# Optimization experiments

Hardware: AMD Instinct MI355X
Metric: run time of the kernel (lower is better)

The kernel has to match this reference:

```python
import jax, jax.numpy as jnp
import numpy as np

N = 8192      # n_nodes
F = 512       # input feature dim
MLP = 512     # mlp_channels
C = 256       # output channels
H = 2         # MLP layers
KPI = 10      # power iterations
ALPHA = 0.1   # teleport probability


def setup_inputs() -> dict:
    key = jax.random.key(0)
    ks = jax.random.split(key, 10)
    features = jax.random.normal(ks[0], (N, F), dtype=jnp.float32)
    # dense normalized-adjacency surrogate: nonnegative, rows ~ sum to 1
    fltr = jax.random.uniform(ks[1], (N, N), dtype=jnp.float32) * (2.0 / N)
    s = 1.0 / np.sqrt(F)
    W_mlp0 = jax.random.normal(ks[2], (F, MLP), dtype=jnp.float32) * s
    b_mlp0 = jnp.zeros((MLP,), dtype=jnp.float32)
    W_mlp1 = jax.random.normal(ks[3], (MLP, MLP), dtype=jnp.float32) * (1.0 / np.sqrt(MLP))
    b_mlp1 = jnp.zeros((MLP,), dtype=jnp.float32)
    W_out = jax.random.normal(ks[4], (MLP, C), dtype=jnp.float32) * (1.0 / np.sqrt(MLP))
    b_out = jnp.zeros((C,), dtype=jnp.float32)
    return {"features": features, "fltr": fltr,
            "W_mlp0": W_mlp0, "b_mlp0": b_mlp0,
            "W_mlp1": W_mlp1, "b_mlp1": b_mlp1,
            "W_out": W_out, "b_out": b_out}


def reference(features, fltr, W_mlp0, b_mlp0, W_mlp1, b_mlp1, W_out, b_out):
    # MLP stage: per layer -> X = relu( A @ (X W + b) )   (dropout_rate = 0)
    x = features
    for W, b in ((W_mlp0, b_mlp0), (W_mlp1, b_mlp1)):
        x = jnp.matmul(fltr, jnp.matmul(x, W) + b)  # [N, MLP]
        x = jax.nn.relu(x)
    # output projection
    z0 = jnp.matmul(x, W_out) + b_out  # [N, C]
    # K-step APPNP power iteration: Z <- (1-alpha) A Z + alpha Z0
    def step(z, _):
        z = (1.0 - ALPHA) * jnp.matmul(fltr, z) + ALPHA * z0
        return z, None
    z, _ = jax.lax.scan(step, z0, None, length=KPI)
    return jax.nn.softmax(z, axis=-1)
```

## Files before the change

kernel.cpp:

```cpp
#include <hip/hip_runtime.h>

typedef unsigned short u16;
typedef __attribute__((ext_vector_type(8))) short bf16x8;
typedef __attribute__((ext_vector_type(4))) float f32x4;

__device__ __forceinline__ float bf2f(u16 u) {
    union { unsigned i; float f; } v; v.i = ((unsigned)u) << 16; return v.f;
}
__device__ __forceinline__ u16 f2bf(float f) {
    union { float f; unsigned i; } v; v.f = f;
    unsigned r = v.i + 0x7FFFu + ((v.i >> 16) & 1u);
    return (u16)(r >> 16);
}

#define GL2LDS(g, l) __builtin_amdgcn_global_load_lds(                         \
    (const __attribute__((address_space(1))) void*)(g),                        \
    (__attribute__((address_space(3))) void*)(l), 16, 0, 0)

template<int EPI, int AFP32>
__global__ __launch_bounds__(256, 4)
void gemm_bt(const void* __restrict__ Ap, int lda,
             const u16* __restrict__ Bt, int ldb,
             int KB,
             void* __restrict__ outp,
             const void* __restrict__ aux,
             int ldout, int NC)
{
    __shared__ u16 aL[128 * 64];
    __shared__ u16 bL[128 * 64];

    const int t = threadIdx.x;
    const int wid = t >> 6, lane = t & 63;
    const int quad = lane >> 4, l15 = lane & 15, l7 = lane & 7;
    const int m0 = blockIdx.x * 128, n0 = blockIdx.y * 128;
    const int sk = blockIdx.z;
    const int k0 = sk * KB * 64;

    f32x4 acc[4][4];
    const f32x4 z4 = {0.f, 0.f, 0.f, 0.f};
#pragma unroll
    for (int i = 0; i < 4; ++i)
#pragma unroll
        for (int j = 0; j < 4; ++j) acc[i][j] = z4;

    const int wm = (wid >> 1) * 64, wn = (wid & 1) * 64;

    if (AFP32 == 0) {
        const char* pa[4]; const char* pb[4]; int lo[4];
#pragma unroll
        for (int i = 0; i < 4; ++i) {
            int flat = i * 4096 + wid * 1024 + lane * 16;
            int row  = flat >> 7;
            int csrc = ((flat >> 4) & 7) ^ (row & 7);
            pa[i] = (const char*)Ap + ((size_t)(m0 + row) * lda + k0) * 2 + csrc * 16;
            pb[i] = (const char*)Bt + ((size_t)(n0 + row) * ldb + k0) * 2 + csrc * 16;
            lo[i] = i * 4096 + wid * 1024;
        }
        for (int kb = 0; kb < KB; ++kb) {
#pragma unroll
            for (int i = 0; i < 4; ++i) GL2LDS(pa[i], (char*)aL + lo[i]);
#pragma unroll
            for (int i = 0; i < 4; ++i) GL2LDS(pb[i], (char*)bL + lo[i]);
#pragma unroll
            for (int i = 0; i < 4; ++i) { pa[i] += 128; pb[i] += 128; }
            __syncthreads();
#pragma unroll
            for (int ks = 0; ks < 2; ++ks) {
                const int cr = ((ks * 4 + quad) ^ l7) * 8;
                bf16x8 av[4], bv[4];
#pragma unroll
                for (int mi = 0; mi < 4; ++mi)
                    av[mi] = *(const bf16x8*)(aL + (wm + mi * 16 + l15) * 64 + cr);
#pragma unroll
                for (int ni = 0; ni < 4; ++ni)
                    bv[ni] = *(const bf16x8*)(bL + (wn + ni * 16 + l15) * 64 + cr);
#pragma unroll
                for (int mi = 0; mi < 4; ++mi)
#pragma unroll
                    for (int ni = 0; ni < 4; ++ni)
                        acc[mi][ni] = __builtin_amdgcn_mfma_f32_16x16x32_bf16(
                            av[mi], bv[ni], acc[mi][ni], 0, 0, 0);
            }
            __syncthreads();
        }
    } else {
        for (int kb = 0; kb < KB; ++kb) {
            const int kbase = k0 + kb * 64;
#pragma unroll
            for (int i = 0; i < 4; ++i) {
                int flat = i * 4096 + t * 16;
                int row  = flat >> 7;
                int col  = (flat & 127) >> 1;
                bf16x8 v = *(const bf16x8*)(Bt + (size_t)(n0 + row) * ldb + kbase + col);
                *(bf16x8*)(bL + row * 64 + col) = v;
            }
            const float* Af = (const float*)Ap;
#pragma unroll
            for (int j = 0; j < 8; ++j) {
                int f = j * 256 + t;
                int r = f >> 4, c = (f & 15) * 4;
                float4 v = *(const float4*)(Af + (size_t)(m0 + r) * lda + kbase + c);
                ushort4 o;
                o.x = f2bf(v.x); o.y = f2bf(v.y);
                o.z = f2bf(v.z); o.w = f2bf(v.w);
                *(ushort4*)(aL + r * 64 + c) = o;
            }
            __syncthreads();
#pragma unroll
            for (int ks = 0; ks < 2; ++ks) {
                const int cr = (ks * 4 + quad) * 8;
                bf16x8 av[4], bv[4];
#pragma unroll
                for (int mi = 0; mi < 4; ++mi)
                    av[mi] = *(const bf16x8*)(aL + (wm + mi * 16 + l15) * 64 + cr);
#pragma unroll
                for (int ni = 0; ni < 4; ++ni)
                    bv[ni] = *(const bf16x8*)(bL + (wn + ni * 16 + l15) * 64 + cr);
#pragma unroll
                for (int mi = 0; mi < 4; ++mi)
#pragma unroll
                    for (int ni = 0; ni < 4; ++ni)
                        acc[mi][ni] = __builtin_amdgcn_mfma_f32_16x16x32_bf16(
                            av[mi], bv[ni], acc[mi][ni], 0, 0, 0);
            }
            __syncthreads();
        }
    }

    if (EPI == 0) {
#pragma unroll
        for (int ni = 0; ni < 4; ++ni) {
            int n = n0 + wn + ni * 16 + l15;
            float bvv = ((const float*)aux)[n];
            u16* ob = (u16*)outp + (size_t)n * ldout;
#pragma unroll
            for (int mi = 0; mi < 4; ++mi) {
                int m = m0 + wm + mi * 16 + quad * 4;
                ushort4 o;
                o.x = f2bf(acc[mi][ni][0] + bvv);
                o.y = f2bf(acc[mi][ni][1] + bvv);
                o.z = f2bf(acc[mi][ni][2] + bvv);
                o.w = f2bf(acc[mi][ni][3] + bvv);
                *(ushort4*)(ob + m) = o;
            }
        }
    } else if (EPI == 2) {
#pragma unroll
        for (int ni = 0; ni < 4; ++ni) {
            int n = n0 + wn + ni * 16 + l15;
            u16* ob = (u16*)outp + ((size_t)(sk * NC + n)) * 8192;
#pragma unroll
            for (int mi = 0; mi < 4; ++mi) {
                int m = m0 + wm + mi * 16 + quad * 4;
                ushort4 o;
                o.x = f2bf(acc[mi][ni][0]);
                o.y = f2bf(acc[mi][ni][1]);
                o.z = f2bf(acc[mi][ni][2]);
                o.w = f2bf(acc[mi][ni][3]);
                *(ushort4*)(ob + m) = o;
            }
        }
    } else if (EPI == 3) {
#pragma unroll
        for (int ni = 0; ni < 4; ++ni) {
            int n = n0 + wn + ni * 16 + l15;
            const u16* zrow = (const u16*)aux + (size_t)n * 8192;
            u16* ob = (u16*)outp + (size_t)n * ldout;
#pragma unroll
            for (int mi = 0; mi < 4; ++mi) {
                int m = m0 + wm + mi * 16 + quad * 4;
                ushort4 z0 = *(const ushort4*)(zrow + m);
                ushort4 o;
                o.x = f2bf(0.9f * acc[mi][ni][0] + 0.1f * bf2f(z0.x));
                o.y = f2bf(0.9f * acc[mi][ni][1] + 0.1f * bf2f(z0.y));
                o.z = f2bf(0.9f * acc[mi][ni][2] + 0.1f * bf2f(z0.z));
                o.w = f2bf(0.9f * acc[mi][ni][3] + 0.1f * bf2f(z0.w));
                *(ushort4*)(ob + m) = o;
            }
        }
    } else {
        u16* ob = (u16*)outp;
#pragma unroll
        for (int mi = 0; mi < 4; ++mi) {
            int m = m0 + wm + mi * 16 + quad * 4;
#pragma unroll
            for (int ni = 0; ni < 4; ++ni) {
                int n = n0 + wn + ni * 16 + l15;
#pragma unroll
                for (int r = 0; r < 4; ++r)
                    ob[(size_t)(m + r) * ldout + n] = f2bf(fmaxf(acc[mi][ni][r], 0.0f));
            }
        }
    }
}

__global__ __launch_bounds__(256)
void cvt_f2b_k(const float* __restrict__ in, u16* __restrict__ out, long n4)
{
    long i = (long)blockIdx.x * 256 + threadIdx.x;
    long stride = (long)gridDim.x * 256;
    for (; i < n4; i += stride) {
        float4 v = ((const float4*)in)[i];
        ushort4 o;
        o.x = f2bf(v.x); o.y = f2bf(v.y); o.z = f2bf(v.z); o.w = f2bf(v.w);
        ((ushort4*)out)[i] = o;
    }
}

__global__ __launch_bounds__(256)
void transpose_cvt_k(const float* __restrict__ in, u16* __restrict__ out,
                     int R, int C)
{
    __shared__ u16 tile[32][33];
    int tx = threadIdx.x, ty = threadIdx.y;
    int x = blockIdx.x * 32 + tx;
    int y0 = blockIdx.y * 32 + ty;
#pragma unroll
    for (int j = 0; j < 32; j += 8)
        tile[ty + j][tx] = f2bf(in[(size_t)(y0 + j) * C + x]);
    __syncthreads();
    int x2 = blockIdx.y * 32 + tx;
    int y2 = blockIdx.x * 32 + ty;
#pragma unroll
    for (int j = 0; j < 32; j += 8)
        out[(size_t)(y2 + j) * R + x2] = tile[tx][ty + j];
}

template<int S>
__global__ __launch_bounds__(256)
void combine_bias_k(const u16* __restrict__ part, const float* __restrict__ bias,
                    u16* __restrict__ out, long NROW)
{
    const size_t Sz = (size_t)NROW * 8192;
    size_t e = ((size_t)blockIdx.x * 256 + threadIdx.x) * 4;
    int n = (int)(e >> 13);
    float b = bias[n];
    ushort4 p0 = *(const ushort4*)(part + e);
    float sx = bf2f(p0.x), sy = bf2f(p0.y), sz = bf2f(p0.z), sw = bf2f(p0.w);
#pragma unroll
    for (int i = 1; i < S; ++i) {
        ushort4 v = *(const ushort4*)(part + (size_t)i * Sz + e);
        sx += bf2f(v.x); sy += bf2f(v.y); sz += bf2f(v.z); sw += bf2f(v.w);
    }
    ushort4 o;
    o.x = f2bf(sx + b); o.y = f2bf(sy + b);
    o.z = f2bf(sz + b); o.w = f2bf(sw + b);
    *(ushort4*)(out + e) = o;
}

template<int S>
__global__ __launch_bounds__(256)
void combine_mlp_k(const u16* __restrict__ part, u16* __restrict__ y)
{
    __shared__ u16 L[64][68];
    const int t = threadIdx.x;
    const int mb = blockIdx.x * 64;
    const int nb = blockIdx.y * 64;
    const size_t Sz = (size_t)512 * 8192;
#pragma unroll
    for (int i = 0; i < 4; ++i) {
        int flat = i * 256 + t;
        int nl = flat >> 4;
        int mq = flat & 15;
        const u16* p0 = part + (size_t)(nb + nl) * 8192 + mb + mq * 4;
        ushort4 a4 = *(const ushort4*)p0;
        float ax = bf2f(a4.x), ay = bf2f(a4.y), az = bf2f(a4.z), aw = bf2f(a4.w);
#pragma unroll
        for (int s = 1; s < S; ++s) {
            ushort4 v = *(const ushort4*)(p0 + (size_t)s * Sz);
            ax += bf2f(v.x); ay += bf2f(v.y); az += bf2f(v.z); aw += bf2f(v.w);
        }
        ushort4 o;
        o.x = f2bf(fmaxf(ax, 0.f)); o.y = f2bf(fmaxf(ay, 0.f));
        o.z = f2bf(fmaxf(az, 0.f)); o.w = f2bf(fmaxf(aw, 0.f));
        *(ushort4*)&L[nl][mq * 4] = o;
    }
    __syncthreads();
#pragma unroll
    for (int i = 0; i < 4; ++i) {
        int flat = i * 256 + t;
        int ml  = flat >> 4;
        int nl4 = (flat & 15) * 4;
        ushort4 o;
        o.x = L[nl4 + 0][ml]; o.y = L[nl4 + 1][ml];
        o.z = L[nl4 + 2][ml]; o.w = L[nl4 + 3][ml];
        *(ushort4*)(y + (size_t)(mb + ml) * 512 + nb + nl4) = o;
    }
}

template<int S>
__global__ __launch_bounds__(256)
void combine_iter_k(const u16* __restrict__ part, const u16* __restrict__ z0T,
                    u16* __restrict__ zT)
{
    const size_t Sz = (size_t)256 * 8192;
    size_t e = ((size_t)blockIdx.x * 256 + threadIdx.x) * 4;
    ushort4 p0 = *(const ushort4*)(part + e);
    float ax = bf2f(p0.x), ay = bf2f(p0.y), az = bf2f(p0.z), aw = bf2f(p0.w);
#pragma unroll
    for (int s = 1; s < S; ++s) {
        ushort4 v = *(const ushort4*)(part + (size_t)s * Sz + e);
        ax += bf2f(v.x); ay += bf2f(v.y); az += bf2f(v.z); aw += bf2f(v.w);
    }
    ushort4 z0 = *(const ushort4*)(z0T + e);
    ushort4 o;
    o.x = f2bf(0.9f * ax + 0.1f * bf2f(z0.x));
    o.y = f2bf(0.9f * ay + 0.1f * bf2f(z0.y));
    o.z = f2bf(0.9f * az + 0.1f * bf2f(z0.z));
    o.w = f2bf(0.9f * aw + 0.1f * bf2f(z0.w));
    *(ushort4*)(zT + e) = o;
}

__global__ __launch_bounds__(256)
void softmax_k(const u16* __restrict__ zT, float* __restrict__ out)
{
    __shared__ u16 L[64][260];
    const int t = threadIdx.x;
    const int m0 = blockIdx.x * 64;
    const int tx = t & 15, ty = t >> 4;
#pragma unroll
    for (int i = 0; i < 16; ++i) {
        int n = i * 16 + ty;
        ushort4 v = *(const ushort4*)(zT + (size_t)n * 8192 + m0 + tx * 4);
        L[tx * 4 + 0][n] = v.x; L[tx * 4 + 1][n] = v.y;
        L[tx * 4 + 2][n] = v.z; L[tx * 4 + 3][n] = v.w;
    }
    __syncthreads();
    const int wid = t >> 6, lane = t & 63;
    for (int r = 0; r < 16; ++r) {
        int mm = wid * 16 + r;
        ushort4 u = *(const ushort4*)(&L[mm][lane * 4]);
        float f0 = bf2f(u.x), f1 = bf2f(u.y), f2 = bf2f(u.z), f3 = bf2f(u.w);
        float mx = fmaxf(fmaxf(f0, f1), fmaxf(f2, f3));
#pragma unroll
        for (int off = 32; off > 0; off >>= 1) mx = fmaxf(mx, __shfl_xor(mx, off));
        float e0 = __expf(f0 - mx), e1 = __expf(f1 - mx);
        float e2 = __expf(f2 - mx), e3 = __expf(f3 - mx);
        float s = e0 + e1 + e2 + e3;
#pragma unroll
        for (int off = 32; off > 0; off >>= 1) s += __shfl_xor(s, off);
        float inv = 1.0f / s;
        float4 o;
        o.x = e0 * inv; o.y = e1 * inv; o.z = e2 * inv; o.w = e3 * inv;
        *(float4*)(out + (size_t)(m0 + mm) * 256 + lane * 4) = o;
    }
}

extern "C" void kernel_launch(void* const* d_in, const int* in_sizes, int n_in,
                              void* d_out, int out_size, void* d_ws, size_t ws_size,
                              hipStream_t stream)
{
    const float* features = (const float*)d_in[0];
    const float* fltr     = (const float*)d_in[1];
    const float* W0       = (const float*)d_in[2];
    const float* b0       = (const float*)d_in[3];
    const float* W1       = (const float*)d_in[4];
    const float* b1       = (const float*)d_in[5];
    const float* Wo       = (const float*)d_in[6];
    const float* bo       = (const float*)d_in[7];

    dim3 tb(32, 8);

    char* p = (char*)d_ws;
    u16* fB  = (u16*)p;  p += (size_t)8192 * 512 * 2;
    u16* W0T = (u16*)p;  p += (size_t)512 * 512 * 2;
    u16* W1T = (u16*)p;  p += (size_t)512 * 512 * 2;
    u16* WoT = (u16*)p;  p += (size_t)256 * 512 * 2;
    u16* z0T = (u16*)p;  p += (size_t)256 * 8192 * 2;
    u16* zA  = (u16*)p;  p += (size_t)256 * 8192 * 2;
    u16* zB  = (u16*)p;  p += (size_t)256 * 8192 * 2;
    u16* tT  = (u16*)p;  p += (size_t)512 * 8192 * 2;
    u16* y   = (u16*)p;  p += (size_t)8192 * 512 * 2;
    u16* part = (u16*)p; p += (size_t)4 * 512 * 8192 * 2;
    size_t base_need = (size_t)(p - (char*)d_ws);
    u16* fltrB = (u16*)p;
    size_t full_need = base_need + (size_t)8192 * 8192 * 2;

    if (ws_size >= full_need) {
        cvt_f2b_k<<<2048, 256, 0, stream>>>(fltr, fltrB, (long)8192 * 8192 / 4);
        cvt_f2b_k<<<512, 256, 0, stream>>>(features, fB, (long)8192 * 512 / 4);
        transpose_cvt_k<<<dim3(16, 16), tb, 0, stream>>>(W0, W0T, 512, 512);
        transpose_cvt_k<<<dim3(16, 16), tb, 0, stream>>>(W1, W1T, 512, 512);
        transpose_cvt_k<<<dim3(8, 16),  tb, 0, stream>>>(Wo, WoT, 512, 256);

        gemm_bt<0, 0><<<dim3(64, 4, 1), 256, 0, stream>>>(fB, 512, W0T, 512, 8,
                                                          tT, b0, 8192, 0);
        gemm_bt<2, 0><<<dim3(64, 4, 2), 256, 0, stream>>>(fltrB, 8192, tT, 8192,
                                                          64, part, nullptr, 0, 512);
        combine_mlp_k<2><<<dim3(128, 8), 256, 0, stream>>>(part, y);
        gemm_bt<0, 0><<<dim3(64, 4, 1), 256, 0, stream>>>(y, 512, W1T, 512, 8,
                                                          tT, b1, 8192, 0);
        gemm_bt<2, 0><<<dim3(64, 4, 2), 256, 0, stream>>>(fltrB, 8192, tT, 8192,
                                                          64, part, nullptr, 0, 512);
        combine_mlp_k<2><<<dim3(128, 8), 256, 0, stream>>>(part, y);
        gemm_bt<0, 0><<<dim3(64, 2, 1), 256, 0, stream>>>(y, 512, WoT, 512, 8,
                                                          z0T, bo, 8192, 0);
        const u16* src = z0T;
        for (int it = 0; it < 10; ++it) {
            u16* dst = (it & 1) ? zB : zA;
            gemm_bt<2, 0><<<dim3(64, 2, 4), 256, 0, stream>>>(fltrB, 8192, src,
                                                              8192, 32, part,
                                                              nullptr, 0, 256);
            combine_iter_k<4><<<2048, 256, 0, stream>>>(part, z0T, dst);
            src = dst;
        }
        softmax_k<<<128, 256, 0, stream>>>(src, (float*)d_out);
    } else if (ws_size >= base_need) {
        cvt_f2b_k<<<512, 256, 0, stream>>>(features, fB, (long)8192 * 512 / 4);
        transpose_cvt_k<<<dim3(16, 16), tb, 0, stream>>>(W0, W0T, 512, 512);
        transpose_cvt_k<<<dim3(16, 16), tb, 0, stream>>>(W1, W1T, 512, 512);
        transpose_cvt_k<<<dim3(8, 16),  tb, 0, stream>>>(Wo, WoT, 512, 256);

        gemm_bt<2, 0><<<dim3(64, 4, 2), 256, 0, stream>>>(fB, 512, W0T, 512, 4,
                                                          part, nullptr, 0, 512);
        combine_bias_k<2><<<4096, 256, 0, stream>>>(part, b0, tT, 512);
        gemm_bt<2, 1><<<dim3(64, 4, 4), 256, 0, stream>>>(fltr, 8192, tT, 8192,
                                                          32, part, nullptr, 0, 512);
        combine_mlp_k<4><<<dim3(128, 8), 256, 0, stream>>>(part, y);
        gemm_bt<2, 0><<<dim3(64, 4, 2), 256, 0, stream>>>(y, 512, W1T, 512, 4,
                                                          part, nullptr, 0, 512);
        combine_bias_k<2><<<4096, 256, 0, stream>>>(part, b1, tT, 512);
        gemm_bt<2, 1><<<dim3(64, 4, 4), 256, 0, stream>>>(fltr, 8192, tT, 8192,
                                                          32, part, nullptr, 0, 512);
        combine_mlp_k<4><<<dim3(128, 8), 256, 0, stream>>>(part, y);
        gemm_bt<2, 0><<<dim3(64, 2, 4), 256, 0, stream>>>(y, 512, WoT, 512, 2,
                                                          part, nullptr, 0, 256);
        combine_bias_k<4><<<2048, 256, 0, stream>>>(part, bo, z0T, 256);
        const u16* src = z0T;
        for (int it = 0; it < 10; ++it) {
            u16* dst = (it & 1) ? zB : zA;
            gemm_bt<2, 1><<<dim3(64, 2, 8), 256, 0, stream>>>(fltr, 8192, src,
                                                              8192, 16, part,
                                                              nullptr, 0, 256);
            combine_iter_k<8><<<2048, 256, 0, stream>>>(part, z0T, dst);
            src = dst;
        }
        softmax_k<<<128, 256, 0, stream>>>(src, (float*)d_out);
    } else {
        char* w = (char*)d_ws;
        u16* fW0T = (u16*)w;  w += (size_t)512 * 512 * 2;
        u16* fW1T = (u16*)w;  w += (size_t)512 * 512 * 2;
        u16* fWoT = (u16*)w;  w += (size_t)256 * 512 * 2;
        u16* fz0T = (u16*)w;  w += (size_t)256 * 8192 * 2;
        char* rb = w;
        u16* ftT = (u16*)rb;
        u16* fy  = (u16*)(rb + (size_t)512 * 8192 * 2);
        u16* fzA = (u16*)rb;
        u16* fzB = (u16*)(rb + (size_t)256 * 8192 * 2);

        transpose_cvt_k<<<dim3(16, 16), tb, 0, stream>>>(W0, fW0T, 512, 512);
        transpose_cvt_k<<<dim3(16, 16), tb, 0, stream>>>(W1, fW1T, 512, 512);
        transpose_cvt_k<<<dim3(8, 16),  tb, 0, stream>>>(Wo, fWoT, 512, 256);
        gemm_bt<0, 1><<<dim3(64, 4), 256, 0, stream>>>(features, 512, fW0T, 512, 8,
                                                       ftT, b0, 8192, 0);
        gemm_bt<1, 1><<<dim3(64, 4), 256, 0, stream>>>(fltr, 8192, ftT, 8192, 128,
                                                       fy, nullptr, 512, 0);
        gemm_bt<0, 0><<<dim3(64, 4), 256, 0, stream>>>(fy, 512, fW1T, 512, 8,
                                                       ftT, b1, 8192, 0);
        gemm_bt<1, 1><<<dim3(64, 4), 256, 0, stream>>>(fltr, 8192, ftT, 8192, 128,
                                                       fy, nullptr, 512, 0);
        gemm_bt<0, 0><<<dim3(64, 2), 256, 0, stream>>>(fy, 512, fWoT, 512, 8,
                                                       fz0T, bo, 8192, 0);
        const u16* src = fz0T;
        for (int it = 0; it < 10; ++it) {
            u16* dst = (it & 1) ? fzB : fzA;
            gemm_bt<3, 1><<<dim3(64, 2), 256, 0, stream>>>(fltr, 8192, src, 8192,
                                                           128, dst, fz0T, 8192, 0);
            src = dst;
        }
        softmax_k<<<128, 256, 0, stream>>>(src, (float*)d_out);
    }
}
```

Measured before the change: 1.115 ms.

## Add 256x256-tile 8-wave GEMM with phased LDS pipeline for adjacency matmuls

After: 1.057 ms. 5.1% less time.

```diff
diff --git a/kernel.cpp b/kernel.cpp
--- a/kernel.cpp
+++ b/kernel.cpp
@@ -193,6 +193,125 @@
         }
     }
 }
+
+#define PHASE_MFMA(MH)                                                        \
+    asm volatile("s_waitcnt lgkmcnt(0)" ::: "memory");                        \
+    __builtin_amdgcn_sched_barrier(0);                                        \
+    __builtin_amdgcn_s_setprio(1);                                            \
+    _Pragma("unroll")                                                         \
+    for (int mi = 0; mi < 4; ++mi)                                            \
+        _Pragma("unroll")                                                     \
+        for (int ni = 0; ni < 4; ++ni)                                        \
+            acc[(MH) * 4 + mi][ni] = __builtin_amdgcn_mfma_f32_16x16x32_bf16( \
+                av[mi], bv[ni], acc[(MH) * 4 + mi][ni], 0, 0, 0);             \
+    __builtin_amdgcn_s_setprio(0);
+
+__global__ __launch_bounds__(512, 2)
+void gemm256(const u16* __restrict__ A, int lda,
+             const u16* __restrict__ Bt, int ldb,
+             int nt,
+             u16* __restrict__ part, int NC)
+{
+    __shared__ u16 lds[65536];
+    const int t = threadIdx.x;
+    const int wid = t >> 6, lane = t & 63;
+    const int quad = lane >> 4, l15 = lane & 15, l7 = lane & 7;
+    const int wr = wid >> 2, wc = wid & 3;
+    const int m0 = blockIdx.x * 256, n0 = blockIdx.y * 256;
+    const int sk = blockIdx.z;
+    const size_t k0 = (size_t)sk * nt * 64;
+
+    f32x4 acc[8][4];
+    const f32x4 z4 = {0.f, 0.f, 0.f, 0.f};
+#pragma unroll
+    for (int i = 0; i < 8; ++i)
+#pragma unroll
+        for (int j = 0; j < 4; ++j) acc[i][j] = z4;
+
+    const char* pa[2][2]; const char* pb[2][2]; int uo[2][2];
+#pragma unroll
+    for (int h = 0; h < 2; ++h)
+#pragma unroll
+        for (int j = 0; j < 2; ++j) {
+            int p = j * 8192 + wid * 1024 + lane * 16;
+            int row = p >> 7;
+            int csrc = ((p >> 4) & 7) ^ (row & 7);
+            pa[h][j] = (const char*)A +
+                ((size_t)(m0 + h * 128 + row) * lda + k0) * 2 + csrc * 16;
+            pb[h][j] = (const char*)Bt +
+                ((size_t)(n0 + h * 128 + row) * ldb + k0) * 2 + csrc * 16;
+            uo[h][j] = h * 16384 + j * 8192 + wid * 1024;
+        }
+#define STGA(h, d) { GL2LDS(pa[h][0], (char*)lds + (d) * 32768 + uo[h][0]);    \
+                     GL2LDS(pa[h][1], (char*)lds + (d) * 32768 + uo[h][1]);    \
+                     pa[h][0] += 128; pa[h][1] += 128; }
+#define STGB(h, d) { GL2LDS(pb[h][0], (char*)lds + 65536 + (d) * 32768 + uo[h][0]); \
+                     GL2LDS(pb[h][1], (char*)lds + 65536 + (d) * 32768 + uo[h][1]); \
+                     pb[h][0] += 128; pb[h][1] += 128; }
+
+    STGA(0, 0); STGA(1, 0); STGB(0, 0); STGB(1, 0);
+    STGA(0, 1); STGA(1, 1); STGB(0, 1); STGB(1, 1);
+    asm volatile("s_waitcnt vmcnt(8)" ::: "memory");
+    __builtin_amdgcn_s_barrier();
+
+    const int cb0 = ((quad ^ l7) << 4);
+    const int cb1 = (((4 + quad) ^ l7) << 4);
+    const int aro = l15 * 128;
+    const int bro = ((wc & 1) * 64 + l15) * 128;
+
+    for (int g = 0; g < nt; ++g) {
+        const int d = g & 1;
+        const char* Ab = (const char*)lds + d * 32768 + wr * 16384 + aro;
+        const char* Bb = (const char*)lds + 65536 + d * 32768 + (wc >> 1) * 16384 + bro;
+        bf16x8 av[4], bv[4];
+#pragma unroll
+        for (int i = 0; i < 4; ++i) bv[i] = *(const bf16x8*)(Bb + i * 2048 + cb0);
+#pragma unroll
+        for (int i = 0; i < 4; ++i) av[i] = *(const bf16x8*)(Ab + i * 2048 + cb0);
+        if (g >= 1 && g + 1 < nt) STGA(0, d ^ 1);
+        __builtin_amdgcn_s_barrier();
+        PHASE_MFMA(0)
+        __builtin_amdgcn_s_barrier();
+#pragma unroll
+        for (int i = 0; i < 4; ++i) av[i] = *(const bf16x8*)(Ab + (4 + i) * 2048 + cb0);
+        if (g >= 1 && g + 1 < nt) STGA(1, d ^ 1);
+        __builtin_amdgcn_s_barrier();
+        PHASE_MFMA(1)
+        __builtin_amdgcn_s_barrier();
+#pragma unroll
+        for (int i = 0; i < 4; ++i) bv[i] = *(const bf16x8*)(Bb + i * 2048 + cb1);
+#pragma unroll
+        for (int i = 0; i < 4; ++i) av[i] = *(const bf16x8*)(Ab + i * 2048 + cb1);
+        __builtin_amdgcn_s_barrier();
+        PHASE_MFMA(0)
+        __builtin_amdgcn_s_barrier();
+#pragma unroll
+        for (int i = 0; i < 4; ++i) av[i] = *(const bf16x8*)(Ab + (4 + i) * 2048 + cb1);
+        if (g + 2 < nt) { STGB(0, d); STGB(1, d); }
+        __builtin_amdgcn_s_barrier();
+        PHASE_MFMA(1)
+        asm volatile("s_waitcnt vmcnt(4)" ::: "memory");
+        __builtin_amdgcn_s_barrier();
+    }
+
+#pragma unroll
+    for (int ni = 0; ni < 4; ++ni) {
+        int n = n0 + wc * 64 + ni * 16 + l15;
+        u16* ob = part + ((size_t)(sk * NC + n)) * 8192;
+#pragma unroll
+        for (int mi = 0; mi < 8; ++mi) {
+            int m = m0 + wr * 128 + mi * 16 + quad * 4;
+            ushort4 o;
+            o.x = f2bf(acc[mi][ni][0]);
+            o.y = f2bf(acc[mi][ni][1]);
+            o.z = f2bf(acc[mi][ni][2]);
+            o.w = f2bf(acc[mi][ni][3]);
+            *(ushort4*)(ob + m) = o;
+        }
+    }
+}
+#undef STGA
+#undef STGB
 
 __global__ __launch_bounds__(256)
 void cvt_f2b_k(const float* __restrict__ in, u16* __restrict__ out, long n4)
@@ -385,23 +504,22 @@
 
         gemm_bt<0, 0><<<dim3(64, 4, 1), 256, 0, stream>>>(fB, 512, W0T, 512, 8,
                                                           tT, b0, 8192, 0);
-        gemm_bt<2, 0><<<dim3(64, 4, 2), 256, 0, stream>>>(fltrB, 8192, tT, 8192,
-                                                          64, part, nullptr, 0, 512);
-        combine_mlp_k<2><<<dim3(128, 8), 256, 0, stream>>>(part, y);
+        gemm256<<<dim3(32, 2, 4), 512, 0, stream>>>(fltrB, 8192, tT, 8192, 32,
+                                                    part, 512);
+        combine_mlp_k<4><<<dim3(128, 8), 256, 0, stream>>>(part, y);
         gemm_bt<0, 0><<<dim3(64, 4, 1), 256, 0, stream>>>(y, 512, W1T, 512, 8,
                                                           tT, b1, 8192, 0);
-        gemm_bt<2, 0><<<dim3(64, 4, 2), 256, 0, stream>>>(fltrB, 8192, tT, 8192,
-                                                          64, part, nullptr, 0, 512);
-        combine_mlp_k<2><<<dim3(128, 8), 256, 0, stream>>>(part, y);
+        gemm256<<<dim3(32, 2, 4), 512, 0, stream>>>(fltrB, 8192, tT, 8192, 32,
+                                                    part, 512);
+        combine_mlp_k<4><<<dim3(128, 8), 256, 0, stream>>>(part, y);
         gemm_bt<0, 0><<<dim3(64, 2, 1), 256, 0, stream>>>(y, 512, WoT, 512, 8,
                                                           z0T, bo, 8192, 0);
         const u16* src = z0T;
         for (int it = 0; it < 10; ++it) {
             u16* dst = (it & 1) ? zB : zA;
-            gemm_bt<2, 0><<<dim3(64, 2, 4), 256, 0, stream>>>(fltrB, 8192, src,
-                                                              8192, 32, part,
-                                                              nullptr, 0, 256);
-            combine_iter_k<4><<<2048, 256, 0, stream>>>(part, z0T, dst);
+            gemm256<<<dim3(32, 1, 8), 512, 0, stream>>>(fltrB, 8192, src, 8192,
+                                                        16, part, 256);
+            combine_iter_k<8><<<2048, 256, 0, stream>>>(part, z0T, dst);
             src = dst;
         }
         softmax_k<<<128, 256, 0, stream>>>(src, (float*)d_out);
```

## Add 128x256-tile, 8-wave, triple-buffered GEMM for large adjacency products

Applied to the files above, without the earlier changes.

After: 1.068 ms. 1.04x faster.

```diff
diff --git a/kernel.cpp b/kernel.cpp
--- a/kernel.cpp
+++ b/kernel.cpp
@@ -193,6 +193,127 @@
         }
     }
 }
+
+__global__ __launch_bounds__(512, 1)
+void gemm_bp(const u16* __restrict__ A, int lda,
+             const u16* __restrict__ Bt, int ldb,
+             int nt,
+             u16* __restrict__ part, int NC)
+{
+    __shared__ u16 lds[73728];
+    const int t = threadIdx.x;
+    const int wid = t >> 6, lane = t & 63;
+    const int quad = lane >> 4, l15 = lane & 15, l7 = lane & 7;
+    const int wr = wid >> 2, wc = wid & 3;
+    const int m0 = blockIdx.x * 128, n0 = blockIdx.y * 256;
+    const int sk = blockIdx.z;
+    const size_t k0 = (size_t)sk * nt * 64;
+
+    f32x4 acc[4][4];
+    const f32x4 z4 = {0.f, 0.f, 0.f, 0.f};
+#pragma unroll
+    for (int i = 0; i < 4; ++i)
+#pragma unroll
+        for (int j = 0; j < 4; ++j) acc[i][j] = z4;
+
+    const char* pa[2]; int ua[2];
+    const char* pb[4]; int ub[4];
+#pragma unroll
+    for (int j = 0; j < 2; ++j) {
+        int p = j * 8192 + t * 16;
+        int row = p >> 7;
+        int csrc = ((p >> 4) & 7) ^ (row & 7);
+        pa[j] = (const char*)A + ((size_t)(m0 + row) * lda + k0) * 2 + csrc * 16;
+        ua[j] = j * 8192 + wid * 1024;
+    }
+#pragma unroll
+    for (int j = 0; j < 4; ++j) {
+        int p = j * 8192 + t * 16;
+        int row = p >> 7;
+        int csrc = ((p >> 4) & 7) ^ (row & 7);
+        pb[j] = (const char*)Bt + ((size_t)(n0 + row) * ldb + k0) * 2 + csrc * 16;
+        ub[j] = j * 8192 + wid * 1024;
+    }
+#define STGA_BP(d) { GL2LDS(pa[0], (char*)lds + (d) * 16384 + ua[0]);          \
+                     GL2LDS(pa[1], (char*)lds + (d) * 16384 + ua[1]);          \
+                     pa[0] += 128; pa[1] += 128; }
+#define STGB_BP(d) { GL2LDS(pb[0], (char*)lds + 49152 + (d) * 32768 + ub[0]);  \
+                     GL2LDS(pb[1], (char*)lds + 49152 + (d) * 32768 + ub[1]);  \
+                     GL2LDS(pb[2], (char*)lds + 49152 + (d) * 32768 + ub[2]);  \
+                     GL2LDS(pb[3], (char*)lds + 49152 + (d) * 32768 + ub[3]);  \
+                     pb[0] += 128; pb[1] += 128; pb[2] += 128; pb[3] += 128; }
+
+    STGA_BP(0); STGB_BP(0); STGA_BP(1); STGB_BP(1);
+    asm volatile("s_waitcnt vmcnt(6)" ::: "memory");
+    __builtin_amdgcn_s_barrier();
+
+    const int aro = (wr * 64 + l15) * 128;
+    const int bro = (wc * 64 + l15) * 128;
+    const int cb0 = ((quad ^ l7) << 4);
+    const int cb1 = (((4 + quad) ^ l7) << 4);
+
+    int d = 0, dn = 2;
+    for (int g = 0; g < nt; ++g) {
+        const char* Ab = (const char*)lds + d * 16384 + aro;
+        const char* Bb = (const char*)lds + 49152 + d * 32768 + bro;
+        bf16x8 av[4], bv[4];
+#pragma unroll
+        for (int i = 0; i < 4; ++i) bv[i] = *(const bf16x8*)(Bb + i * 2048 + cb0);
+#pragma unroll
+        for (int i = 0; i < 4; ++i) av[i] = *(const bf16x8*)(Ab + i * 2048 + cb0);
+        if (g + 2 < nt) { STGA_BP(dn); STGB_BP(dn); }
+        __builtin_amdgcn_s_barrier();
+        asm volatile("s_waitcnt lgkmcnt(0)" ::: "memory");
+        __builtin_amdgcn_sched_barrier(0);
+        __builtin_amdgcn_s_setprio(1);
+#pragma unroll
+        for (int mi = 0; mi < 4; ++mi)
+#pragma unroll
+            for (int ni = 0; ni < 4; ++ni)
+                acc[mi][ni] = __builtin_amdgcn_mfma_f32_16x16x32_bf16(
+                    av[mi], bv[ni], acc[mi][ni], 0, 0, 0);
+        __builtin_amdgcn_s_setprio(0);
+        __builtin_amdgcn_s_barrier();
+#pragma unroll
+        for (int i = 0; i < 4; ++i) bv[i] = *(const bf16x8*)(Bb + i * 2048 + cb1);
+#pragma unroll
+        for (int i = 0; i < 4; ++i) av[i] = *(const bf16x8*)(Ab + i * 2048 + cb1);
+        __builtin_amdgcn_s_barrier();
+        asm volatile("s_waitcnt lgkmcnt(0)" ::: "memory");
+        __builtin_amdgcn_sched_barrier(0);
+        __builtin_amdgcn_s_setprio(1);
+#pragma unroll
+        for (int mi = 0; mi < 4; ++mi)
+#pragma unroll
+            for (int ni = 0; ni < 4; ++ni)
+                acc[mi][ni] = __builtin_amdgcn_mfma_f32_16x16x32_bf16(
+                    av[mi], bv[ni], acc[mi][ni], 0, 0, 0);
+        __builtin_amdgcn_s_setprio(0);
+        if (g + 2 < nt) { asm volatile("s_waitcnt vmcnt(6)" ::: "memory"); }
+        else            { asm volatile("s_waitcnt vmcnt(0)" ::: "memory"); }
+        __builtin_amdgcn_s_barrier();
+        d  = (d  + 1 == 3) ? 0 : d  + 1;
+        dn = (dn + 1 == 3) ? 0 : dn + 1;
+    }
+
+#pragma unroll
+    for (int ni = 0; ni < 4; ++ni) {
+        int n = n0 + wc * 64 + ni * 16 + l15;
+        u16* ob = part + ((size_t)(sk * NC + n)) * 8192;
+#pragma unroll
+        for (int mi = 0; mi < 4; ++mi) {
+            int m = m0 + wr * 64 + mi * 16 + quad * 4;
+            ushort4 o;
+            o.x = f2bf(acc[mi][ni][0]);
+            o.y = f2bf(acc[mi][ni][1]);
+            o.z = f2bf(acc[mi][ni][2]);
+            o.w = f2bf(acc[mi][ni][3]);
+            *(ushort4*)(ob + m) = o;
+        }
+    }
+}
+#undef STGA_BP
+#undef STGB_BP
 
 __global__ __launch_bounds__(256)
 void cvt_f2b_k(const float* __restrict__ in, u16* __restrict__ out, long n4)
@@ -385,22 +506,21 @@
 
         gemm_bt<0, 0><<<dim3(64, 4, 1), 256, 0, stream>>>(fB, 512, W0T, 512, 8,
                                                           tT, b0, 8192, 0);
-        gemm_bt<2, 0><<<dim3(64, 4, 2), 256, 0, stream>>>(fltrB, 8192, tT, 8192,
-                                                          64, part, nullptr, 0, 512);
+        gemm_bp<<<dim3(64, 2, 2), 512, 0, stream>>>(fltrB, 8192, tT, 8192, 64,
+                                                    part, 512);
         combine_mlp_k<2><<<dim3(128, 8), 256, 0, stream>>>(part, y);
         gemm_bt<0, 0><<<dim3(64, 4, 1), 256, 0, stream>>>(y, 512, W1T, 512, 8,
                                                           tT, b1, 8192, 0);
-        gemm_bt<2, 0><<<dim3(64, 4, 2), 256, 0, stream>>>(fltrB, 8192, tT, 8192,
-                                                          64, part, nullptr, 0, 512);
+        gemm_bp<<<dim3(64, 2, 2), 512, 0, stream>>>(fltrB, 8192, tT, 8192, 64,
+                                                    part, 512);
         combine_mlp_k<2><<<dim3(128, 8), 256, 0, stream>>>(part, y);
         gemm_bt<0, 0><<<dim3(64, 2, 1), 256, 0, stream>>>(y, 512, WoT, 512, 8,
                                                           z0T, bo, 8192, 0);
         const u16* src = z0T;
         for (int it = 0; it < 10; ++it) {
             u16* dst = (it & 1) ? zB : zA;
-            gemm_bt<2, 0><<<dim3(64, 2, 4), 256, 0, stream>>>(fltrB, 8192, src,
-                                                              8192, 32, part,
-                                                              nullptr, 0, 256);
+            gemm_bp<<<dim3(64, 1, 4), 512, 0, stream>>>(fltrB, 8192, src, 8192,
+                                                        32, part, 256);
             combine_iter_k<4><<<2048, 256, 0, stream>>>(part, z0T, dst);
             src = dst;
         }
```
